# Optimization experiments

Hardware: AMD Instinct MI355X
Metric: run time of the kernel (lower is better)

The kernel has to match this reference:

```python
import jax, jax.numpy as jnp
import numpy as np

B, I, H = 16384, 512, 512


def _linear_params(key, out_dim, in_dim):
    kw, kb = jax.random.split(key)
    bound = 1.0 / np.sqrt(in_dim)
    W = jax.random.uniform(kw, (out_dim, in_dim), jnp.float32, -bound, bound)
    b = jax.random.uniform(kb, (out_dim,), jnp.float32, -bound, bound)
    return W, b


def setup_inputs() -> dict:
    key = jax.random.key(0)
    ks = jax.random.split(key, 12)
    x = jax.random.normal(ks[0], (B, I), jnp.float32)
    h_prev = jax.random.normal(ks[1], (B, H), jnp.float32)
    c_prev = jax.random.normal(ks[2], (B, H), jnp.float32)
    W_xi, b_xi = _linear_params(ks[3], H, I)
    W_hi, b_hi = _linear_params(ks[4], H, H)
    W_xf, b_xf = _linear_params(ks[5], H, I)
    W_hf, b_hf = _linear_params(ks[6], H, H)
    W_xc, b_xc = _linear_params(ks[7], H, I)
    W_hc, b_hc = _linear_params(ks[8], H, H)
    W_xo, b_xo = _linear_params(ks[9], H, I)
    W_ho, b_ho = _linear_params(ks[10], H, H)
    W_e, b_e = _linear_params(ks[11], H, I + H)
    return dict(x=x, h_prev=h_prev, c_prev=c_prev,
                W_xi=W_xi, b_xi=b_xi, W_hi=W_hi, b_hi=b_hi,
                W_xf=W_xf, b_xf=b_xf, W_hf=W_hf, b_hf=b_hf,
                W_xc=W_xc, b_xc=b_xc, W_hc=W_hc, b_hc=b_hc,
                W_xo=W_xo, b_xo=b_xo, W_ho=W_ho, b_ho=b_ho,
                W_e=W_e, b_e=b_e)


def reference(x, h_prev, c_prev,
              W_xi, b_xi, W_hi, b_hi,
              W_xf, b_xf, W_hf, b_hf,
              W_xc, b_xc, W_hc, b_hc,
              W_xo, b_xo, W_ho, b_ho,
              W_e, b_e):
    # Batch the 4 input-to-hidden projections into one GEMM and the 4
    # hidden-to-hidden projections into another (same math as 8 Linears).
    Wx = jnp.concatenate([W_xi, W_xf, W_xc, W_xo], axis=0)   # [4H, I]
    bx = jnp.concatenate([b_xi, b_xf, b_xc, b_xo], axis=0)   # [4H]
    Wh = jnp.concatenate([W_hi, W_hf, W_hc, W_ho], axis=0)   # [4H, H]
    bh = jnp.concatenate([b_hi, b_hf, b_hc, b_ho], axis=0)
    gates = (x @ Wx.T + bx) + (h_prev @ Wh.T + bh)            # [B, 4H]
    gi, gf, gc, go = jnp.split(gates, 4, axis=-1)
    i = jax.nn.sigmoid(gi)
    f = jax.nn.sigmoid(gf)
    g = jnp.tanh(gc)
    o = jax.nn.sigmoid(go)
    c = f * c_prev + i * g
    # exp gate: Linear on [x, h_prev] -> tanh -> exp; split W_e to avoid concat
    We_x, We_h = W_e[:, :x.shape[-1]], W_e[:, x.shape[-1]:]
    exp_factor = jnp.exp(jnp.tanh(x @ We_x.T + h_prev @ We_h.T + b_e))
    h = o * jnp.tanh(c) * exp_factor
    return (h, c)
```

## Files before the change

### kernel.cpp

```cpp
#include <hip/hip_runtime.h>
#include <stdint.h>

#define Bsz 16384
#define Hh  512
#define Kd  1024
#define BM  256
#define NT  32

#define BUFB 26624

typedef __attribute__((ext_vector_type(8))) short bf16x8;
typedef __attribute__((ext_vector_type(4))) float f32x4;
typedef __attribute__((ext_vector_type(8))) unsigned short u16x8;

__device__ __forceinline__ unsigned short f2bf(float f) {
    union { float f; unsigned u; } v; v.f = f;
    unsigned u = v.u;
    return (unsigned short)((u + 0x7fffu + ((u >> 16) & 1u)) >> 16);
}
__device__ __forceinline__ float fast_tanh(float x) {
    float e = __expf(2.f * x);
    return (e - 1.f) / (e + 1.f);
}
__device__ __forceinline__ float fast_sigmoid(float x) {
    return 1.f / (1.f + __expf(-x));
}

__global__ void pack_A(const float* __restrict__ x, const float* __restrict__ h,
                       unsigned short* __restrict__ A) {
    const long total = (long)Bsz * Kd / 8;
    for (long i = (long)blockIdx.x * blockDim.x + threadIdx.x; i < total;
         i += (long)gridDim.x * blockDim.x) {
        int  l    = (int)(i & 63);
        long blk  = i >> 6;
        int  u    = (int)(blk & 7);
        int  t    = (int)((blk >> 3) & 31);
        long mblk = blk >> 8;
        long row  = mblk * 128 + u * 16 + (l & 15);
        int  k0   = t * 32 + ((l >> 4) << 3);
        const float* src = (k0 < 512) ? (x + row * 512 + k0)
                                      : (h + row * 512 + (k0 - 512));
        float4 f0 = *(const float4*)(src);
        float4 f1 = *(const float4*)(src + 4);
        u16x8 o;
        o[0]=f2bf(f0.x); o[1]=f2bf(f0.y); o[2]=f2bf(f0.z); o[3]=f2bf(f0.w);
        o[4]=f2bf(f1.x); o[5]=f2bf(f1.y); o[6]=f2bf(f1.z); o[7]=f2bf(f1.w);
        *(u16x8*)(A + (i << 3)) = o;
    }
}

__global__ void pack_B(const float* __restrict__ Wxi, const float* __restrict__ Whi,
                       const float* __restrict__ Wxf, const float* __restrict__ Whf,
                       const float* __restrict__ Wxc, const float* __restrict__ Whc,
                       const float* __restrict__ Wxo, const float* __restrict__ Who,
                       const float* __restrict__ We,
                       const float* __restrict__ bxi, const float* __restrict__ bhi,
                       const float* __restrict__ bxf, const float* __restrict__ bhf,
                       const float* __restrict__ bxc, const float* __restrict__ bhc,
                       const float* __restrict__ bxo, const float* __restrict__ bho,
                       const float* __restrict__ be,
                       unsigned short* __restrict__ Bp, float* __restrict__ bias) {
    const long id = (long)blockIdx.x * blockDim.x + threadIdx.x;
    if (id < 327680) {
        int blk = (int)(id >> 6);
        int l   = (int)(id & 63);
        int kh  = blk & 1;
        int kt  = (blk >> 1) & 15;
        int rest = blk >> 5;
        int g    = rest % 5;
        int jgrp = rest / 5;
        int j  = jgrp * 16 + (l & 15);
        int k0 = kt * 64 + kh * 32 + ((l >> 4) << 3);
        const float* src;
        if (g == 4) {
            src = We + (long)j * 1024 + k0;
        } else {
            const float* Wx = (g == 0) ? Wxi : (g == 1) ? Wxf : (g == 2) ? Wxc : Wxo;
            const float* Wh = (g == 0) ? Whi : (g == 1) ? Whf : (g == 2) ? Whc : Who;
            src = (k0 < 512) ? (Wx + (long)j * 512 + k0)
                             : (Wh + (long)j * 512 + (k0 - 512));
        }
        float4 f0 = *(const float4*)(src);
        float4 f1 = *(const float4*)(src + 4);
        u16x8 o;
        o[0]=f2bf(f0.x); o[1]=f2bf(f0.y); o[2]=f2bf(f0.z); o[3]=f2bf(f0.w);
        o[4]=f2bf(f1.x); o[5]=f2bf(f1.y); o[6]=f2bf(f1.z); o[7]=f2bf(f1.w);
        *(u16x8*)(Bp + (long)blk * 512 + l * 8) = o;
    }
    if (id < 2560) {
        int row = (int)id;
        int g = row >> 9, j = row & 511;
        float b;
        if (g == 4) b = be[j];
        else {
            const float* bx = (g == 0) ? bxi : (g == 1) ? bxf : (g == 2) ? bxc : bxo;
            const float* bh = (g == 0) ? bhi : (g == 1) ? bhf : (g == 2) ? bhc : bho;
            b = bx[j] + bh[j];
        }
        bias[row] = b;
    }
}

#define GL16(g, l) __builtin_amdgcn_global_load_lds( \
    (const __attribute__((address_space(1))) unsigned int*)(g), \
    (__attribute__((address_space(3))) unsigned int*)(l), 16, 0, 0)

#define VM_I(n)    asm volatile("s_waitcnt vmcnt(" #n ")" ::: "memory")
#define VM(n)      VM_I(n)
#define BARRIER()  asm volatile("s_barrier" ::: "memory")

#define MF(a, b, c) __builtin_amdgcn_mfma_f32_16x16x32_bf16(a, b, c, 0, 0, 0)

#define RDALL(BO) do { \
    _Pragma("unroll") \
    for (int m_ = 0; m_ < 8; ++m_) \
        af[m_] = *(const bf16x8*)(aRP + (BO) + m_ * 1024); \
    _Pragma("unroll") \
    for (int g_ = 0; g_ < 5; ++g_) \
        bq[g_] = *(const bf16x8*)(bRP + (BO) + g_ * 1024); \
} while (0)

#define MFMA40() do { \
    __builtin_amdgcn_s_setprio(1); \
    _Pragma("unroll") \
    for (int g_ = 0; g_ < 5; ++g_) \
        _Pragma("unroll") \
        for (int m_ = 0; m_ < 8; ++m_) \
            acc[m_][g_] = MF(af[m_], bq[g_], acc[m_][g_]); \
    __builtin_amdgcn_s_setprio(0); \
} while (0)

#define SG7(SO, T) do { \
    GL16(sg0 + (long)(T) * st0, lds_raw + (SO) + ld0); \
    GL16(sg1 + (long)(T) * st1, lds_raw + (SO) + ld1); \
    GL16(sg2 + (long)(T) * st2, lds_raw + (SO) + ld2); \
    GL16(sg3 + (long)(T) * st3, lds_raw + (SO) + ld3); \
    GL16(sg4 + (long)(T) * st4, lds_raw + (SO) + ld4); \
    GL16(sg5 + (long)(T) * st5, lds_raw + (SO) + ld5); \
    GL16(sg6 + (long)(T) * st6, lds_raw + (SO) + ld6); \
} while (0)

#define TILE(T, RBO, SBO, STG, WN, SYNC) do { \
    RDALL(RBO); \
    if (STG) SG7(SBO, (T) + 2); \
    MFMA40(); \
    if (SYNC) { VM(WN); BARRIER(); } \
} while (0)

__global__ __launch_bounds__(256, 1)
void xlstm_gemm(const unsigned short* __restrict__ Apk,
                const unsigned short* __restrict__ Bp,
                const float* __restrict__ bias,
                const float* __restrict__ c_prev,
                float* __restrict__ out) {
    __shared__ __align__(16) unsigned char lds_raw[3 * BUFB];

    const int tid  = threadIdx.x;
    const int wid  = tid >> 6;
    const int lane = tid & 63;
    const int wm   = wid >> 1;
    const int wj   = wid & 1;
    const int fr   = lane & 15;
    const int q    = lane >> 4;

    const int orig = blockIdx.x;
    const int wg   = (orig & 7) * 128 + (orig >> 3);
    const int Mblk = wg >> 4;
    const int Jblk = wg & 15;
    const long brow = (long)Mblk * BM;

    f32x4 acc[8][5];
#pragma unroll
    for (int m = 0; m < 8; ++m)
#pragma unroll
        for (int g = 0; g < 5; ++g)
#pragma unroll
            for (int r = 0; r < 4; ++r) acc[m][g][r] = 0.f;

    bf16x8 af[8];
    bf16x8 bq[5];

    const unsigned char* aRP = lds_raw + wm * 8192 + lane * 16;
    const unsigned char* bRP = lds_raw + 16384 + wj * 5120 + lane * 16;

    const unsigned short *sg0, *sg1, *sg2, *sg3, *sg4, *sg5, *sg6;
    int st0, st1, st2, st3, st4, st5, st6;
    int ld0, ld1, ld2, ld3, ld4, ld5, ld6;
#define SLOT_INIT(s) do { \
    int u_ = (s) * 4 + wid; if (u_ >= 26) u_ -= 26; \
    if (u_ < 16) { \
        long mb_ = (long)(Mblk * 2 + (u_ >> 3)); \
        sg##s = Apk + mb_ * 131072 + (u_ & 7) * 512 + lane * 8; \
        st##s = 4096; \
    } else { \
        int b_ = u_ - 16; int wjg_ = b_ / 5; int g_ = b_ - 5 * wjg_; \
        sg##s = Bp + (long)(Jblk * 2 + wjg_) * 81920 + g_ * 16384 + lane * 8; \
        st##s = 512; \
    } \
    ld##s = u_ * 1024 + lane * 16; \
} while (0)
    SLOT_INIT(0); SLOT_INIT(1); SLOT_INIT(2); SLOT_INIT(3);
    SLOT_INIT(4); SLOT_INIT(5); SLOT_INIT(6);
#undef SLOT_INIT

    SG7(0, 0);
    SG7(BUFB, 1);
    VM(7);
    BARRIER();

    for (int t = 0; t < 30; t += 3) {
        TILE(t,     0 * BUFB, 2 * BUFB, 1, 7, 1);
        TILE(t + 1, 1 * BUFB, 0 * BUFB, 1, 7, 1);
        TILE(t + 2, 2 * BUFB, 1 * BUFB, 1, 7, 1);
    }
    TILE(30, 0 * BUFB, 0, 0, 0, 1);
    TILE(31, 1 * BUFB, 0, 0, 0, 0);

    const int j = Jblk * 32 + wj * 16 + fr;
    const float bi_ = bias[j];
    const float bf_ = bias[512 + j];
    const float bc_ = bias[1024 + j];
    const float bo_ = bias[1536 + j];
    const float be_ = bias[2048 + j];
    const long mbase = brow + wm * 128 + (q << 2);
#pragma unroll
    for (int m = 0; m < 8; ++m) {
#pragma unroll
        for (int r = 0; r < 4; ++r) {
            long row = mbase + m * 16 + r;
            float gi = acc[m][0][r] + bi_;
            float gf = acc[m][1][r] + bf_;
            float gc = acc[m][2][r] + bc_;
            float go = acc[m][3][r] + bo_;
            float ge = acc[m][4][r] + be_;
            float iv = fast_sigmoid(gi);
            float fv = fast_sigmoid(gf);
            float gv = fast_tanh(gc);
            float ov = fast_sigmoid(go);
            float ef = __expf(fast_tanh(ge));
            float cp = c_prev[row * 512 + j];
            float cv = fv * cp + iv * gv;
            float hv = ov * fast_tanh(cv) * ef;
            out[row * 512 + j] = hv;
            out[(long)Bsz * 512 + row * 512 + j] = cv;
        }
    }
}

extern "C" void kernel_launch(void* const* d_in, const int* in_sizes, int n_in,
                              void* d_out, int out_size, void* d_ws, size_t ws_size,
                              hipStream_t stream) {
    const float* x      = (const float*)d_in[0];
    const float* h_prev = (const float*)d_in[1];
    const float* c_prev = (const float*)d_in[2];
    const float* Wxi = (const float*)d_in[3];
    const float* bxi = (const float*)d_in[4];
    const float* Whi = (const float*)d_in[5];
    const float* bhi = (const float*)d_in[6];
    const float* Wxf = (const float*)d_in[7];
    const float* bxf = (const float*)d_in[8];
    const float* Whf = (const float*)d_in[9];
    const float* bhf = (const float*)d_in[10];
    const float* Wxc = (const float*)d_in[11];
    const float* bxc = (const float*)d_in[12];
    const float* Whc = (const float*)d_in[13];
    const float* bhc = (const float*)d_in[14];
    const float* Wxo = (const float*)d_in[15];
    const float* bxo = (const float*)d_in[16];
    const float* Who = (const float*)d_in[17];
    const float* bho = (const float*)d_in[18];
    const float* We  = (const float*)d_in[19];
    const float* be  = (const float*)d_in[20];

    unsigned short* Abf  = (unsigned short*)d_ws;
    unsigned short* Bp   = (unsigned short*)((char*)d_ws + 33554432);
    float*          bias = (float*)((char*)d_ws + 33554432 + 5242880);

    pack_A<<<2048, 256, 0, stream>>>(x, h_prev, Abf);
    pack_B<<<1280, 256, 0, stream>>>(Wxi, Whi, Wxf, Whf, Wxc, Whc, Wxo, Who, We,
                                     bxi, bhi, bxf, bhf, bxc, bhc, bxo, bho, be,
                                     Bp, bias);
    xlstm_gemm<<<1024, 256, 0, stream>>>(Abf, Bp, bias, c_prev, (float*)d_out);
}
```

Measured before the change: 147.7 us.

## Split GEMM block work across 16 waves with smaller per-wave tiles

The fused LSTM GEMM kernel now launches 1024 threads (16 waves) per block instead of 256. Each wave computes a 32-row by 5-gate sub-tile, so it holds 10 accumulators rather than 40, and issues 2 global-to-LDS loads per stage instead of 7. The aim is more waves in flight to hide memory and LDS latency and lower register pressure. The cost is less reuse of each fragment loaded from LDS: there are more LDS reads per MFMA, and a few LDS slots are written redundantly by two waves.

```diff
diff --git a/kernel.cpp b/kernel.cpp
--- a/kernel.cpp
+++ b/kernel.cpp
@@ -5,6 +5,7 @@
 #define Hh  512
 #define Kd  1024
 #define BM  256
+#define BNJ 32
 #define NT  32
 
 #define BUFB 26624
@@ -111,43 +112,39 @@
 
 #define MF(a, b, c) __builtin_amdgcn_mfma_f32_16x16x32_bf16(a, b, c, 0, 0, 0)
 
-#define RDALL(BO) do { \
-    _Pragma("unroll") \
-    for (int m_ = 0; m_ < 8; ++m_) \
-        af[m_] = *(const bf16x8*)(aRP + (BO) + m_ * 1024); \
-    _Pragma("unroll") \
-    for (int g_ = 0; g_ < 5; ++g_) \
-        bq[g_] = *(const bf16x8*)(bRP + (BO) + g_ * 1024); \
-} while (0)
-
-#define MFMA40() do { \
+#define RD7(BO) do { \
+    af0 = *(const bf16x8*)(aRP + (BO) + 0 * 1024); \
+    af1 = *(const bf16x8*)(aRP + (BO) + 1 * 1024); \
+    bq0 = *(const bf16x8*)(bRP + (BO) + 0 * 1024); \
+    bq1 = *(const bf16x8*)(bRP + (BO) + 1 * 1024); \
+    bq2 = *(const bf16x8*)(bRP + (BO) + 2 * 1024); \
+    bq3 = *(const bf16x8*)(bRP + (BO) + 3 * 1024); \
+    bq4 = *(const bf16x8*)(bRP + (BO) + 4 * 1024); \
+} while (0)
+
+#define MFMA10() do { \
     __builtin_amdgcn_s_setprio(1); \
-    _Pragma("unroll") \
-    for (int g_ = 0; g_ < 5; ++g_) \
-        _Pragma("unroll") \
-        for (int m_ = 0; m_ < 8; ++m_) \
-            acc[m_][g_] = MF(af[m_], bq[g_], acc[m_][g_]); \
+    acc[0][0] = MF(af0, bq0, acc[0][0]); acc[0][1] = MF(af1, bq0, acc[0][1]); \
+    acc[1][0] = MF(af0, bq1, acc[1][0]); acc[1][1] = MF(af1, bq1, acc[1][1]); \
+    acc[2][0] = MF(af0, bq2, acc[2][0]); acc[2][1] = MF(af1, bq2, acc[2][1]); \
+    acc[3][0] = MF(af0, bq3, acc[3][0]); acc[3][1] = MF(af1, bq3, acc[3][1]); \
+    acc[4][0] = MF(af0, bq4, acc[4][0]); acc[4][1] = MF(af1, bq4, acc[4][1]); \
     __builtin_amdgcn_s_setprio(0); \
 } while (0)
 
-#define SG7(SO, T) do { \
+#define SG2(SO, T) do { \
     GL16(sg0 + (long)(T) * st0, lds_raw + (SO) + ld0); \
     GL16(sg1 + (long)(T) * st1, lds_raw + (SO) + ld1); \
-    GL16(sg2 + (long)(T) * st2, lds_raw + (SO) + ld2); \
-    GL16(sg3 + (long)(T) * st3, lds_raw + (SO) + ld3); \
-    GL16(sg4 + (long)(T) * st4, lds_raw + (SO) + ld4); \
-    GL16(sg5 + (long)(T) * st5, lds_raw + (SO) + ld5); \
-    GL16(sg6 + (long)(T) * st6, lds_raw + (SO) + ld6); \
 } while (0)
 
 #define TILE(T, RBO, SBO, STG, WN, SYNC) do { \
-    RDALL(RBO); \
-    if (STG) SG7(SBO, (T) + 2); \
-    MFMA40(); \
+    RD7(RBO); \
+    if (STG) SG2(SBO, (T) + 2); \
+    MFMA10(); \
     if (SYNC) { VM(WN); BARRIER(); } \
 } while (0)
 
-__global__ __launch_bounds__(256, 1)
+__global__ __launch_bounds__(1024, 1)
 void xlstm_gemm(const unsigned short* __restrict__ Apk,
                 const unsigned short* __restrict__ Bp,
                 const float* __restrict__ bias,
@@ -169,49 +166,46 @@
     const int Jblk = wg & 15;
     const long brow = (long)Mblk * BM;
 
-    f32x4 acc[8][5];
-#pragma unroll
-    for (int m = 0; m < 8; ++m)
-#pragma unroll
-        for (int g = 0; g < 5; ++g)
-#pragma unroll
-            for (int r = 0; r < 4; ++r) acc[m][g][r] = 0.f;
-
-    bf16x8 af[8];
-    bf16x8 bq[5];
-
-    const unsigned char* aRP = lds_raw + wm * 8192 + lane * 16;
+    f32x4 acc[5][2];
+#pragma unroll
+    for (int g = 0; g < 5; ++g)
+#pragma unroll
+        for (int m = 0; m < 2; ++m)
+#pragma unroll
+            for (int r = 0; r < 4; ++r) acc[g][m][r] = 0.f;
+
+    bf16x8 af0, af1, bq0, bq1, bq2, bq3, bq4;
+
+    const unsigned char* aRP = lds_raw + wm * 2048 + lane * 16;
     const unsigned char* bRP = lds_raw + 16384 + wj * 5120 + lane * 16;
 
-    const unsigned short *sg0, *sg1, *sg2, *sg3, *sg4, *sg5, *sg6;
-    int st0, st1, st2, st3, st4, st5, st6;
-    int ld0, ld1, ld2, ld3, ld4, ld5, ld6;
+    const unsigned short *sg0, *sg1;
+    int st0, st1, ld0, ld1;
 #define SLOT_INIT(s) do { \
-    int u_ = (s) * 4 + wid; if (u_ >= 26) u_ -= 26; \
+    int u_ = wid * 2 + (s); if (u_ >= 26) u_ -= 26; \
     if (u_ < 16) { \
         long mb_ = (long)(Mblk * 2 + (u_ >> 3)); \
         sg##s = Apk + mb_ * 131072 + (u_ & 7) * 512 + lane * 8; \
         st##s = 4096; \
     } else { \
-        int b_ = u_ - 16; int wjg_ = b_ / 5; int g_ = b_ - 5 * wjg_; \
-        sg##s = Bp + (long)(Jblk * 2 + wjg_) * 81920 + g_ * 16384 + lane * 8; \
+        int b_ = u_ - 16; int jg_ = b_ / 5; int g_ = b_ - 5 * jg_; \
+        sg##s = Bp + (long)(Jblk * 2 + jg_) * 81920 + g_ * 16384 + lane * 8; \
         st##s = 512; \
     } \
     ld##s = u_ * 1024 + lane * 16; \
 } while (0)
-    SLOT_INIT(0); SLOT_INIT(1); SLOT_INIT(2); SLOT_INIT(3);
-    SLOT_INIT(4); SLOT_INIT(5); SLOT_INIT(6);
+    SLOT_INIT(0); SLOT_INIT(1);
 #undef SLOT_INIT
 
-    SG7(0, 0);
-    SG7(BUFB, 1);
-    VM(7);
+    SG2(0, 0);
+    SG2(BUFB, 1);
+    VM(2);
     BARRIER();
 
     for (int t = 0; t < 30; t += 3) {
-        TILE(t,     0 * BUFB, 2 * BUFB, 1, 7, 1);
-        TILE(t + 1, 1 * BUFB, 0 * BUFB, 1, 7, 1);
-        TILE(t + 2, 2 * BUFB, 1 * BUFB, 1, 7, 1);
+        TILE(t,     0 * BUFB, 2 * BUFB, 1, 2, 1);
+        TILE(t + 1, 1 * BUFB, 0 * BUFB, 1, 2, 1);
+        TILE(t + 2, 2 * BUFB, 1 * BUFB, 1, 2, 1);
     }
     TILE(30, 0 * BUFB, 0, 0, 0, 1);
     TILE(31, 1 * BUFB, 0, 0, 0, 0);
@@ -222,17 +216,17 @@
     const float bc_ = bias[1024 + j];
     const float bo_ = bias[1536 + j];
     const float be_ = bias[2048 + j];
-    const long mbase = brow + wm * 128 + (q << 2);
-#pragma unroll
-    for (int m = 0; m < 8; ++m) {
+    const long mbase = brow + wm * 32 + (q << 2);
+#pragma unroll
+    for (int m = 0; m < 2; ++m) {
 #pragma unroll
         for (int r = 0; r < 4; ++r) {
             long row = mbase + m * 16 + r;
-            float gi = acc[m][0][r] + bi_;
-            float gf = acc[m][1][r] + bf_;
-            float gc = acc[m][2][r] + bc_;
-            float go = acc[m][3][r] + bo_;
-            float ge = acc[m][4][r] + be_;
+            float gi = acc[0][m][r] + bi_;
+            float gf = acc[1][m][r] + bf_;
+            float gc = acc[2][m][r] + bc_;
+            float go = acc[3][m][r] + bo_;
+            float ge = acc[4][m][r] + be_;
             float iv = fast_sigmoid(gi);
             float fv = fast_sigmoid(gf);
             float gv = fast_tanh(gc);
@@ -280,5 +274,5 @@
     pack_B<<<1280, 256, 0, stream>>>(Wxi, Whi, Wxf, Whf, Wxc, Whc, Wxo, Who, We,
                                      bxi, bhi, bxf, bhf, bxc, bhc, bxo, bho, be,
                                      Bp, bias);
-    xlstm_gemm<<<1024, 256, 0, stream>>>(Abf, Bp, bias, c_prev, (float*)d_out);
-}
+    xlstm_gemm<<<1024, 1024, 0, stream>>>(Abf, Bp, bias, c_prev, (float*)d_out);
+}
```

Measured after the change: 121.6 us. 1.21x faster.

## Split exp-gate GEMM into separate kernel and widen main gate GEMM tiles

Applied to the files above, without the earlier changes.

Moves the exp-gate projection into its own GEMM kernel, which writes exp(tanh(.)) as bf16 to a workspace buffer. The main LSTM gate kernel now uses 512-thread blocks with 256x64 tiles covering the four gates, and reads the precomputed exp factor in its epilogue. The goal is a power-of-two N tile without the odd 5-gate split, plus higher occupancy. In exchange it adds a kernel launch, an extra round trip of a B x H bf16 intermediate through memory, re-reads of the A operand, and bf16 rounding of the exp factor.

```diff
diff --git a/kernel.cpp b/kernel.cpp
--- a/kernel.cpp
+++ b/kernel.cpp
@@ -4,10 +4,7 @@
 #define Bsz 16384
 #define Hh  512
 #define Kd  1024
-#define BM  256
 #define NT  32
-
-#define BUFB 26624
 
 typedef __attribute__((ext_vector_type(8))) short bf16x8;
 typedef __attribute__((ext_vector_type(4))) float f32x4;
@@ -17,6 +14,9 @@
     union { float f; unsigned u; } v; v.f = f;
     unsigned u = v.u;
     return (unsigned short)((u + 0x7fffu + ((u >> 16) & 1u)) >> 16);
+}
+__device__ __forceinline__ float bf2f(unsigned short u) {
+    union { unsigned u; float f; } v; v.u = ((unsigned)u) << 16; return v.f;
 }
 __device__ __forceinline__ float fast_tanh(float x) {
     float e = __expf(2.f * x);
@@ -111,49 +111,14 @@
 
 #define MF(a, b, c) __builtin_amdgcn_mfma_f32_16x16x32_bf16(a, b, c, 0, 0, 0)
 
-#define RDALL(BO) do { \
-    _Pragma("unroll") \
-    for (int m_ = 0; m_ < 8; ++m_) \
-        af[m_] = *(const bf16x8*)(aRP + (BO) + m_ * 1024); \
-    _Pragma("unroll") \
-    for (int g_ = 0; g_ < 5; ++g_) \
-        bq[g_] = *(const bf16x8*)(bRP + (BO) + g_ * 1024); \
-} while (0)
-
-#define MFMA40() do { \
-    __builtin_amdgcn_s_setprio(1); \
-    _Pragma("unroll") \
-    for (int g_ = 0; g_ < 5; ++g_) \
-        _Pragma("unroll") \
-        for (int m_ = 0; m_ < 8; ++m_) \
-            acc[m_][g_] = MF(af[m_], bq[g_], acc[m_][g_]); \
-    __builtin_amdgcn_s_setprio(0); \
-} while (0)
-
-#define SG7(SO, T) do { \
-    GL16(sg0 + (long)(T) * st0, lds_raw + (SO) + ld0); \
-    GL16(sg1 + (long)(T) * st1, lds_raw + (SO) + ld1); \
-    GL16(sg2 + (long)(T) * st2, lds_raw + (SO) + ld2); \
-    GL16(sg3 + (long)(T) * st3, lds_raw + (SO) + ld3); \
-    GL16(sg4 + (long)(T) * st4, lds_raw + (SO) + ld4); \
-    GL16(sg5 + (long)(T) * st5, lds_raw + (SO) + ld5); \
-    GL16(sg6 + (long)(T) * st6, lds_raw + (SO) + ld6); \
-} while (0)
-
-#define TILE(T, RBO, SBO, STG, WN, SYNC) do { \
-    RDALL(RBO); \
-    if (STG) SG7(SBO, (T) + 2); \
-    MFMA40(); \
-    if (SYNC) { VM(WN); BARRIER(); } \
-} while (0)
-
-__global__ __launch_bounds__(256, 1)
-void xlstm_gemm(const unsigned short* __restrict__ Apk,
-                const unsigned short* __restrict__ Bp,
-                const float* __restrict__ bias,
-                const float* __restrict__ c_prev,
-                float* __restrict__ out) {
-    __shared__ __align__(16) unsigned char lds_raw[3 * BUFB];
+#define EBUF 20480
+
+__global__ __launch_bounds__(256, 3)
+void e_gemm(const unsigned short* __restrict__ Apk,
+            const unsigned short* __restrict__ Bp,
+            const float* __restrict__ bias,
+            unsigned short* __restrict__ efb) {
+    __shared__ __align__(16) unsigned char lds_raw[2 * EBUF];
 
     const int tid  = threadIdx.x;
     const int wid  = tid >> 6;
@@ -164,80 +129,221 @@
     const int q    = lane >> 4;
 
     const int orig = blockIdx.x;
-    const int wg   = (orig & 7) * 128 + (orig >> 3);
-    const int Mblk = wg >> 4;
-    const int Jblk = wg & 15;
-    const long brow = (long)Mblk * BM;
-
-    f32x4 acc[8][5];
+    const int wg   = (orig & 7) * 64 + (orig >> 3);
+    const int Mblk = wg & 63;
+    const int Jblk = wg >> 6;
+    const long brow = (long)Mblk * 256;
+
+    f32x4 acc[8][2];
 #pragma unroll
     for (int m = 0; m < 8; ++m)
 #pragma unroll
-        for (int g = 0; g < 5; ++g)
-#pragma unroll
-            for (int r = 0; r < 4; ++r) acc[m][g][r] = 0.f;
-
-    bf16x8 af[8];
-    bf16x8 bq[5];
+        for (int n = 0; n < 2; ++n)
+#pragma unroll
+            for (int r = 0; r < 4; ++r) acc[m][n][r] = 0.f;
+
+    bf16x8 af[8], bq[2];
 
     const unsigned char* aRP = lds_raw + wm * 8192 + lane * 16;
-    const unsigned char* bRP = lds_raw + 16384 + wj * 5120 + lane * 16;
-
-    const unsigned short *sg0, *sg1, *sg2, *sg3, *sg4, *sg5, *sg6;
-    int st0, st1, st2, st3, st4, st5, st6;
-    int ld0, ld1, ld2, ld3, ld4, ld5, ld6;
-#define SLOT_INIT(s) do { \
-    int u_ = (s) * 4 + wid; if (u_ >= 26) u_ -= 26; \
+    const unsigned char* bRP = lds_raw + 16384 + wj * 2048 + lane * 16;
+
+    const unsigned short *sg0, *sg1, *sg2, *sg3, *sg4;
+    int st0, st1, st2, st3, st4, ld0, ld1, ld2, ld3, ld4;
+#define ESLOT(s) do { \
+    int u_ = wid * 5 + (s); \
     if (u_ < 16) { \
         long mb_ = (long)(Mblk * 2 + (u_ >> 3)); \
         sg##s = Apk + mb_ * 131072 + (u_ & 7) * 512 + lane * 8; \
         st##s = 4096; \
+        ld##s = u_ * 1024 + lane * 16; \
     } else { \
-        int b_ = u_ - 16; int wjg_ = b_ / 5; int g_ = b_ - 5 * wjg_; \
-        sg##s = Bp + (long)(Jblk * 2 + wjg_) * 81920 + g_ * 16384 + lane * 8; \
+        int b_ = u_ - 16; \
+        sg##s = Bp + (long)(Jblk * 4 + b_) * 81920 + 4 * 16384 + lane * 8; \
         st##s = 512; \
+        ld##s = 16384 + b_ * 1024 + lane * 16; \
     } \
-    ld##s = u_ * 1024 + lane * 16; \
-} while (0)
-    SLOT_INIT(0); SLOT_INIT(1); SLOT_INIT(2); SLOT_INIT(3);
-    SLOT_INIT(4); SLOT_INIT(5); SLOT_INIT(6);
-#undef SLOT_INIT
-
-    SG7(0, 0);
-    SG7(BUFB, 1);
-    VM(7);
+} while (0)
+    ESLOT(0); ESLOT(1); ESLOT(2); ESLOT(3); ESLOT(4);
+#undef ESLOT
+
+#define ESG5(SO, T) do { \
+    GL16(sg0 + (long)(T) * st0, lds_raw + (SO) + ld0); \
+    GL16(sg1 + (long)(T) * st1, lds_raw + (SO) + ld1); \
+    GL16(sg2 + (long)(T) * st2, lds_raw + (SO) + ld2); \
+    GL16(sg3 + (long)(T) * st3, lds_raw + (SO) + ld3); \
+    GL16(sg4 + (long)(T) * st4, lds_raw + (SO) + ld4); \
+} while (0)
+
+#define ERD(BO) do { \
+    _Pragma("unroll") \
+    for (int m_ = 0; m_ < 8; ++m_) af[m_] = *(const bf16x8*)(aRP + (BO) + m_ * 1024); \
+    bq[0] = *(const bf16x8*)(bRP + (BO) + 0 * 1024); \
+    bq[1] = *(const bf16x8*)(bRP + (BO) + 1 * 1024); \
+} while (0)
+
+#define EMFMA() do { \
+    __builtin_amdgcn_s_setprio(1); \
+    _Pragma("unroll") \
+    for (int n_ = 0; n_ < 2; ++n_) \
+        _Pragma("unroll") \
+        for (int m_ = 0; m_ < 8; ++m_) \
+            acc[m_][n_] = MF(af[m_], bq[n_], acc[m_][n_]); \
+    __builtin_amdgcn_s_setprio(0); \
+} while (0)
+
+#define ETILE(RBO, SBO, T, STG, SYNC) do { \
+    if (STG) ESG5(SBO, (T) + 1); \
+    ERD(RBO); \
+    EMFMA(); \
+    if (SYNC) { VM(0); BARRIER(); } \
+} while (0)
+
+    ESG5(0, 0);
+    VM(0);
     BARRIER();
+    for (int t = 0; t < 30; t += 2) {
+        ETILE(0,    EBUF, t,     1, 1);
+        ETILE(EBUF, 0,    t + 1, 1, 1);
+    }
+    ETILE(0,    EBUF, 30, 1, 1);
+    ETILE(EBUF, 0,    31, 0, 0);
+
+#pragma unroll
+    for (int n = 0; n < 2; ++n) {
+        const int j = (Jblk * 4 + wj * 2 + n) * 16 + fr;
+        const float be_ = bias[2048 + j];
+#pragma unroll
+        for (int m = 0; m < 8; ++m) {
+#pragma unroll
+            for (int r = 0; r < 4; ++r) {
+                long row = brow + wm * 128 + m * 16 + (q << 2) + r;
+                float ge = acc[m][n][r] + be_;
+                efb[row * 512 + j] = f2bf(__expf(fast_tanh(ge)));
+            }
+        }
+    }
+}
+
+#define MBUF 32768
+
+__global__ __launch_bounds__(512, 2)
+void xlstm_gemm(const unsigned short* __restrict__ Apk,
+                const unsigned short* __restrict__ Bp,
+                const float* __restrict__ bias,
+                const float* __restrict__ c_prev,
+                const unsigned short* __restrict__ efb,
+                float* __restrict__ out) {
+    __shared__ __align__(16) unsigned char lds_raw[3 * MBUF];
+
+    const int tid  = threadIdx.x;
+    const int wid  = tid >> 6;
+    const int lane = tid & 63;
+    const int wm   = wid >> 2;
+    const int wj   = wid & 3;
+    const int fr   = lane & 15;
+    const int q    = lane >> 4;
+
+    const int orig = blockIdx.x;
+    const int wg   = (orig & 7) * 64 + (orig >> 3);
+    const int Mblk = wg & 63;
+    const int Jblk = wg >> 6;
+    const long brow = (long)Mblk * 256;
+
+    f32x4 acc[8][4];
+#pragma unroll
+    for (int m = 0; m < 8; ++m)
+#pragma unroll
+        for (int g = 0; g < 4; ++g)
+#pragma unroll
+            for (int r = 0; r < 4; ++r) acc[m][g][r] = 0.f;
+
+    bf16x8 af[8], bq[4];
+
+    const unsigned char* aRP = lds_raw + wm * 8192 + lane * 16;
+    const unsigned char* bRP = lds_raw + 16384 + wj * 4096 + lane * 16;
+
+    const unsigned short *sg0, *sg1, *sg2, *sg3;
+    int st0, st1, st2, st3, ld0, ld1, ld2, ld3;
+#define MSLOT(s) do { \
+    int u_ = wid * 4 + (s); \
+    if (u_ < 16) { \
+        long mb_ = (long)(Mblk * 2 + (u_ >> 3)); \
+        sg##s = Apk + mb_ * 131072 + (u_ & 7) * 512 + lane * 8; \
+        st##s = 4096; \
+        ld##s = u_ * 1024 + lane * 16; \
+    } else { \
+        int b_ = u_ - 16; int jl_ = b_ >> 2; int g_ = b_ & 3; \
+        sg##s = Bp + (long)(Jblk * 4 + jl_) * 81920 + g_ * 16384 + lane * 8; \
+        st##s = 512; \
+        ld##s = 16384 + b_ * 1024 + lane * 16; \
+    } \
+} while (0)
+    MSLOT(0); MSLOT(1); MSLOT(2); MSLOT(3);
+#undef MSLOT
+
+#define MSG4(SO, T) do { \
+    GL16(sg0 + (long)(T) * st0, lds_raw + (SO) + ld0); \
+    GL16(sg1 + (long)(T) * st1, lds_raw + (SO) + ld1); \
+    GL16(sg2 + (long)(T) * st2, lds_raw + (SO) + ld2); \
+    GL16(sg3 + (long)(T) * st3, lds_raw + (SO) + ld3); \
+} while (0)
+
+#define MRD(BO) do { \
+    _Pragma("unroll") \
+    for (int m_ = 0; m_ < 8; ++m_) af[m_] = *(const bf16x8*)(aRP + (BO) + m_ * 1024); \
+    _Pragma("unroll") \
+    for (int g_ = 0; g_ < 4; ++g_) bq[g_] = *(const bf16x8*)(bRP + (BO) + g_ * 1024); \
+} while (0)
+
+#define MMFMA32() do { \
+    __builtin_amdgcn_s_setprio(1); \
+    _Pragma("unroll") \
+    for (int g_ = 0; g_ < 4; ++g_) \
+        _Pragma("unroll") \
+        for (int m_ = 0; m_ < 8; ++m_) \
+            acc[m_][g_] = MF(af[m_], bq[g_], acc[m_][g_]); \
+    __builtin_amdgcn_s_setprio(0); \
+} while (0)
+
+#define MTILE(T, RBO, SBO, STG, WN, SYNC) do { \
+    MRD(RBO); \
+    if (STG) MSG4(SBO, (T) + 2); \
+    MMFMA32(); \
+    if (SYNC) { VM(WN); BARRIER(); } \
+} while (0)
+
+    MSG4(0, 0);
+    MSG4(MBUF, 1);
+    VM(4);
+    BARRIER();
 
     for (int t = 0; t < 30; t += 3) {
-        TILE(t,     0 * BUFB, 2 * BUFB, 1, 7, 1);
-        TILE(t + 1, 1 * BUFB, 0 * BUFB, 1, 7, 1);
-        TILE(t + 2, 2 * BUFB, 1 * BUFB, 1, 7, 1);
-    }
-    TILE(30, 0 * BUFB, 0, 0, 0, 1);
-    TILE(31, 1 * BUFB, 0, 0, 0, 0);
-
-    const int j = Jblk * 32 + wj * 16 + fr;
+        MTILE(t,     0 * MBUF, 2 * MBUF, 1, 4, 1);
+        MTILE(t + 1, 1 * MBUF, 0 * MBUF, 1, 4, 1);
+        MTILE(t + 2, 2 * MBUF, 1 * MBUF, 1, 4, 1);
+    }
+    MTILE(30, 0 * MBUF, 0, 0, 0, 1);
+    MTILE(31, 1 * MBUF, 0, 0, 0, 0);
+
+    const int j = (Jblk * 4 + wj) * 16 + fr;
     const float bi_ = bias[j];
     const float bf_ = bias[512 + j];
     const float bc_ = bias[1024 + j];
     const float bo_ = bias[1536 + j];
-    const float be_ = bias[2048 + j];
-    const long mbase = brow + wm * 128 + (q << 2);
 #pragma unroll
     for (int m = 0; m < 8; ++m) {
 #pragma unroll
         for (int r = 0; r < 4; ++r) {
-            long row = mbase + m * 16 + r;
+            long row = brow + wm * 128 + m * 16 + (q << 2) + r;
             float gi = acc[m][0][r] + bi_;
             float gf = acc[m][1][r] + bf_;
             float gc = acc[m][2][r] + bc_;
             float go = acc[m][3][r] + bo_;
-            float ge = acc[m][4][r] + be_;
             float iv = fast_sigmoid(gi);
             float fv = fast_sigmoid(gf);
             float gv = fast_tanh(gc);
             float ov = fast_sigmoid(go);
-            float ef = __expf(fast_tanh(ge));
+            float ef = bf2f(efb[row * 512 + j]);
             float cp = c_prev[row * 512 + j];
             float cv = fv * cp + iv * gv;
             float hv = ov * fast_tanh(cv) * ef;
@@ -275,10 +381,12 @@
     unsigned short* Abf  = (unsigned short*)d_ws;
     unsigned short* Bp   = (unsigned short*)((char*)d_ws + 33554432);
     float*          bias = (float*)((char*)d_ws + 33554432 + 5242880);
+    unsigned short* efb  = (unsigned short*)((char*)d_ws + 38807552);
 
     pack_A<<<2048, 256, 0, stream>>>(x, h_prev, Abf);
     pack_B<<<1280, 256, 0, stream>>>(Wxi, Whi, Wxf, Whf, Wxc, Whc, Wxo, Who, We,
                                      bxi, bhi, bxf, bhf, bxc, bhc, bxo, bho, be,
                                      Bp, bias);
-    xlstm_gemm<<<1024, 256, 0, stream>>>(Abf, Bp, bias, c_prev, (float*)d_out);
-}
+    e_gemm<<<512, 256, 0, stream>>>(Abf, Bp, bias, efb);
+    xlstm_gemm<<<512, 512, 0, stream>>>(Abf, Bp, bias, c_prev, efb, (float*)d_out);
+}
```

Result: slower. 151.2 us (+2.4%).
